# Performance work log

Hardware: AMD Instinct MI355X
Metric: run time of the kernel (lower is better)

## Reference

```python
import jax, jax.numpy as jnp
import numpy as np

N = 84          # nodes; N*(N-1)/2 == 3486, hardcoded by LayerNorm shapes
P = 3486        # number of pairwise rows
H = 2048        # h_size
EPS = 1e-5


def _gru_cell(x, h, Wih, Whh, bih, bhh):
    # PyTorch GRUCell math. Wih: [3H, in], Whh: [3H, H]
    gi = x @ Wih.T + bih
    gh = h @ Whh.T + bhh
    ir, iz, inew = jnp.split(gi, 3, axis=1)
    hr, hz, hnew = jnp.split(gh, 3, axis=1)
    r = jax.nn.sigmoid(ir + hr)
    z = jax.nn.sigmoid(iz + hz)
    n = jnp.tanh(inew + r * hnew)
    return (1.0 - z) * n + z * h


def _full_ln(x, w, b):
    # nn.LayerNorm([3486, h]) normalizes over BOTH dims jointly (biased var)
    mu = jnp.mean(x)
    var = jnp.mean((x - mu) ** 2)
    return (x - mu) * jax.lax.rsqrt(var + EPS) * w + b


def setup_inputs() -> dict:
    key = jax.random.key(0)
    ks = jax.random.split(key, 22)
    f32 = jnp.float32

    def nrm(k, shape, std):
        return jax.random.normal(k, shape, dtype=f32) * std

    h2 = H // 2
    return {
        "x": nrm(ks[0], (N, 64), 1.0),
        "hid": nrm(ks[1], (P, H), 1.0),
        # GRUCell(64, H) parameters
        "gru_Wih": nrm(ks[2], (3 * H, 64), 1.0 / np.sqrt(64)),
        "gru_Whh": nrm(ks[3], (3 * H, H), 1.0 / np.sqrt(H)),
        "gru_bih": nrm(ks[4], (3 * H,), 0.01),
        "gru_bhh": nrm(ks[5], (3 * H,), 0.01),
        # Linear/LayerNorm stack
        "W1": nrm(ks[6], (H, H), np.sqrt(2.0 / H)),
        "b1": jnp.zeros((H,), f32),
        "ln1_w": jnp.ones((P, H), f32),
        "ln1_b": jnp.zeros((P, H), f32),
        "W2": nrm(ks[7], (h2, H), np.sqrt(2.0 / H)),
        "b2": jnp.zeros((h2,), f32),
        "ln2_w": jnp.ones((P, h2), f32),
        "ln2_b": jnp.zeros((P, h2), f32),
        "W3": nrm(ks[8], (h2, h2), np.sqrt(2.0 / h2)),
        "b3": jnp.zeros((h2,), f32),
        "ln3_w": jnp.ones((P, h2), f32),
        "ln3_b": jnp.zeros((P, h2), f32),
        "W4": nrm(ks[9], (1, h2), np.sqrt(2.0 / h2)),
        "b4": jnp.zeros((1,), f32),
    }


def reference(x, hid, gru_Wih, gru_Whh, gru_bih, gru_bhh,
              W1, b1, ln1_w, ln1_b, W2, b2, ln2_w, ln2_b,
              W3, b3, ln3_w, ln3_b, W4, b4):
    # Pairwise gather: rows ordered (0,1),(0,2),...,(0,N-1),(1,2),... -- matches
    # the torch loop of expand+cat.
    iu, ju = jnp.triu_indices(N, k=1)
    x1 = x[iu]  # [P, 64]
    x2 = x[ju]  # [P, 64]

    h = _gru_cell(x1, hid, gru_Wih, gru_Whh, gru_bih, gru_bhh)
    h = _gru_cell(x2, h, gru_Wih, gru_Whh, gru_bih, gru_bhh)

    h = _full_ln(jax.nn.relu(h @ W1.T + b1), ln1_w, ln1_b)
    h = _full_ln(jax.nn.relu(h @ W2.T + b2), ln2_w, ln2_b)
    h = _full_ln(jax.nn.relu(h @ W3.T + b3), ln3_w, ln3_b)
    vals = jax.nn.sigmoid(h @ W4.T + b4)[:, 0]  # [P]

    # Strict-upper-triangular scatter + symmetrize (equals the torch pad loop)
    M = jnp.zeros((N, N), dtype=vals.dtype).at[iu, ju].set(vals)
    return M + M.T
```

## Files before the change

### kernel.cpp

```cpp
#include <hip/hip_runtime.h>
#include <stdint.h>

#define P_PAIRS 3486
#define NNODES 84
#define HSZ 2048
#define H2SZ 1024
#define G3H 6144
#define LN_EPS 1e-5f

typedef short bf16x8 __attribute__((ext_vector_type(8)));
typedef float f32x4 __attribute__((ext_vector_type(4)));

typedef __attribute__((address_space(3))) unsigned int lds_uint;
typedef __attribute__((address_space(1))) const unsigned int global_cuint;

__device__ __forceinline__ unsigned short f2bf(float f) {
    unsigned int u = __float_as_uint(f);
    return (unsigned short)((u + 0x7fffu + ((u >> 16) & 1u)) >> 16);
}
__device__ __forceinline__ float bf2f(unsigned short s) {
    return __uint_as_float(((unsigned int)s) << 16);
}
__device__ __forceinline__ float sigm(float x) {
    return 1.f / (1.f + expf(-x));
}

#define S_WHH (G3H * HSZ / 4)
#define S_W1  (HSZ * HSZ / 4)
#define S_W2  (H2SZ * HSZ / 4)
#define S_W3  (H2SZ * H2SZ / 4)
#define S_HID (P_PAIRS * HSZ / 4)
#define B0 (S_WHH)
#define B1 (B0 + S_W1)
#define B2 (B1 + S_W2)
#define B3 (B2 + S_W3)
#define B4 (B3 + S_HID)

__device__ __forceinline__ void cvt4(const float4* in, ushort4* out, int i) {
    float4 v = in[i];
    ushort4 o;
    o.x = f2bf(v.x); o.y = f2bf(v.y); o.z = f2bf(v.z); o.w = f2bf(v.w);
    out[i] = o;
}

__global__ void k_prep(const float4* __restrict__ Whh, ushort4* __restrict__ whh_b,
                       const float4* __restrict__ W1, ushort4* __restrict__ w1_b,
                       const float4* __restrict__ W2, ushort4* __restrict__ w2_b,
                       const float4* __restrict__ W3, ushort4* __restrict__ w3_b,
                       const float4* __restrict__ hid, ushort4* __restrict__ hid_b,
                       int* __restrict__ ip, int* __restrict__ jp, float* __restrict__ acc) {
    int idx = blockIdx.x * blockDim.x + threadIdx.x;
    if (idx < 8) acc[idx] = 0.f;
    if (idx < P_PAIRS) {
        int i = 0, rem = idx;
        while (rem >= NNODES - 1 - i) { rem -= NNODES - 1 - i; ++i; }
        ip[idx] = i;
        jp[idx] = i + 1 + rem;
    }
    int stride = gridDim.x * blockDim.x;
    for (; idx < B4; idx += stride) {
        if (idx < B0)      cvt4(Whh, whh_b, idx);
        else if (idx < B1) cvt4(W1, w1_b, idx - B0);
        else if (idx < B2) cvt4(W2, w2_b, idx - B1);
        else if (idx < B3) cvt4(W3, w3_b, idx - B2);
        else               cvt4(hid, hid_b, idx - B3);
    }
}

__global__ void k_gi(const float* __restrict__ x, const float* __restrict__ Wih,
                     const float* __restrict__ bih, float* __restrict__ gi) {
    int idx = blockIdx.x * blockDim.x + threadIdx.x;
    if (idx >= NNODES * G3H) return;
    int node = idx / G3H, n = idx - node * G3H;
    const float* xr = x + node * 64;
    const float* wr = Wih + (size_t)n * 64;
    float s = bih[n];
#pragma unroll
    for (int k = 0; k < 64; ++k) s += xr[k] * wr[k];
    gi[idx] = s;
}

__global__ __launch_bounds__(256)
void k_gemm(const unsigned short* __restrict__ A, const unsigned short* __restrict__ B,
            const float* __restrict__ bias, float* __restrict__ C,
            int M, int N, int K, int relu, float* __restrict__ accg, int redslot) {
    __shared__ __align__(16) unsigned short lsA[2 * 128 * 32];
    __shared__ __align__(16) unsigned short lsB[2 * 128 * 32];
    const int m0 = blockIdx.x * 128;
    const int n0 = blockIdx.y * 128;
    const int tid = threadIdx.x;
    const int lane = tid & 63;
    const int wave = tid >> 6;
    const int wr = (wave >> 1) * 64;
    const int wc = (wave & 1) * 64;
    const int fr = lane & 15;
    const int quad = lane >> 4;
    const int kof = quad * 8;

    f32x4 acc[4][4];
#pragma unroll
    for (int i = 0; i < 4; ++i)
#pragma unroll
        for (int j = 0; j < 4; ++j) {
            f32x4 z = {0.f, 0.f, 0.f, 0.f};
            acc[i][j] = z;
        }

    const int lin0 = (wave * 2) * 1024 + lane * 16;
    const int lin1 = lin0 + 1024;
    const int row0 = lin0 >> 6, col0 = (lin0 & 63) >> 1;
    const int row1 = lin1 >> 6, col1 = (lin1 & 63) >> 1;
    int ga0 = m0 + row0; if (ga0 >= M) ga0 = M - 1;
    int ga1 = m0 + row1; if (ga1 >= M) ga1 = M - 1;
    const int gb0 = n0 + row0, gb1 = n0 + row1;

    const unsigned short* pa0 = A + (size_t)ga0 * K + col0;
    const unsigned short* pa1 = A + (size_t)ga1 * K + col1;
    const unsigned short* pb0 = B + (size_t)gb0 * K + col0;
    const unsigned short* pb1 = B + (size_t)gb1 * K + col1;
    const int ch0 = (wave * 2) * 512;
    const int ch1 = ch0 + 512;

    for (int k0 = 0; k0 < K; k0 += 64) {
        __syncthreads();
#pragma unroll
        for (int h = 0; h < 2; ++h) {
            const int ko = k0 + h * 32;
            const int hb = h * 4096;
            __builtin_amdgcn_global_load_lds((global_cuint*)(pa0 + ko), (lds_uint*)&lsA[hb + ch0], 16, 0, 0);
            __builtin_amdgcn_global_load_lds((global_cuint*)(pa1 + ko), (lds_uint*)&lsA[hb + ch1], 16, 0, 0);
            __builtin_amdgcn_global_load_lds((global_cuint*)(pb0 + ko), (lds_uint*)&lsB[hb + ch0], 16, 0, 0);
            __builtin_amdgcn_global_load_lds((global_cuint*)(pb1 + ko), (lds_uint*)&lsB[hb + ch1], 16, 0, 0);
        }
        __syncthreads();
        bf16x8 av[2][4], bv[2][4];
#pragma unroll
        for (int h = 0; h < 2; ++h) {
            const int hb = h * 4096;
#pragma unroll
            for (int mi = 0; mi < 4; ++mi)
                av[h][mi] = *(const bf16x8*)(&lsA[hb + (wr + mi * 16 + fr) * 32 + kof]);
#pragma unroll
            for (int ni = 0; ni < 4; ++ni)
                bv[h][ni] = *(const bf16x8*)(&lsB[hb + (wc + ni * 16 + fr) * 32 + kof]);
        }
#pragma unroll
        for (int h = 0; h < 2; ++h)
#pragma unroll
            for (int mi = 0; mi < 4; ++mi)
#pragma unroll
                for (int ni = 0; ni < 4; ++ni)
                    acc[mi][ni] = __builtin_amdgcn_mfma_f32_16x16x32_bf16(av[h][mi], bv[h][ni], acc[mi][ni], 0, 0, 0);
    }

    float s1 = 0.f, s2 = 0.f;
#pragma unroll
    for (int mi = 0; mi < 4; ++mi) {
#pragma unroll
        for (int r = 0; r < 4; ++r) {
            int row = m0 + wr + mi * 16 + quad * 4 + r;
            if (row >= M) continue;
#pragma unroll
            for (int ni = 0; ni < 4; ++ni) {
                int col = n0 + wc + ni * 16 + fr;
                float v = acc[mi][ni][r];
                if (bias) v += bias[col];
                if (relu) v = fmaxf(v, 0.f);
                if (redslot >= 0) { s1 += v; s2 += v * v; }
                C[(size_t)row * N + col] = v;
            }
        }
    }

    if (redslot >= 0) {
        __syncthreads();
        float* sm = (float*)lsA;
        sm[tid] = s1;
        sm[256 + tid] = s2;
        __syncthreads();
        for (int o = 128; o > 0; o >>= 1) {
            if (tid < o) {
                sm[tid] += sm[tid + o];
                sm[256 + tid] += sm[256 + tid + o];
            }
            __syncthreads();
        }
        if (tid == 0) {
            atomicAdd(&accg[redslot * 2], sm[0]);
            atomicAdd(&accg[redslot * 2 + 1], sm[256]);
        }
    }
}

__global__ void k_combine(const float4* __restrict__ gi, const float4* __restrict__ gh,
                          const int* __restrict__ pair, const float4* __restrict__ hprev_f,
                          const ushort4* __restrict__ hprev_b,
                          ushort4* __restrict__ hout) {
    int idx = blockIdx.x * blockDim.x + threadIdx.x;
    if (idx >= P_PAIRS * (HSZ / 4)) return;
    int p = idx >> 9;
    int c4 = idx & 511;
    int node = pair[p];
    const float4* gip = gi + (size_t)node * (G3H / 4) + c4;
    const float4* ghp = gh + (size_t)p * (G3H / 4) + c4;
    float4 gir = gip[0],   ghr = ghp[0];
    float4 giz = gip[512], ghz = ghp[512];
    float4 gin = gip[1024], ghn = ghp[1024];
    float hp[4];
    if (hprev_f) {
        float4 h = hprev_f[idx];
        hp[0] = h.x; hp[1] = h.y; hp[2] = h.z; hp[3] = h.w;
    } else {
        ushort4 h = hprev_b[idx];
        hp[0] = bf2f(h.x); hp[1] = bf2f(h.y); hp[2] = bf2f(h.z); hp[3] = bf2f(h.w);
    }
    float ir[4] = {gir.x, gir.y, gir.z, gir.w}, hr[4] = {ghr.x, ghr.y, ghr.z, ghr.w};
    float iz[4] = {giz.x, giz.y, giz.z, giz.w}, hz[4] = {ghz.x, ghz.y, ghz.z, ghz.w};
    float in_[4] = {gin.x, gin.y, gin.z, gin.w}, hn[4] = {ghn.x, ghn.y, ghn.z, ghn.w};
    unsigned short o[4];
#pragma unroll
    for (int q = 0; q < 4; ++q) {
        float r = sigm(ir[q] + hr[q]);
        float z = sigm(iz[q] + hz[q]);
        float nn = tanhf(in_[q] + r * hn[q]);
        o[q] = f2bf((1.f - z) * nn + z * hp[q]);
    }
    ushort4 ov = {o[0], o[1], o[2], o[3]};
    hout[idx] = ov;
}

__global__ void k_lnapply(const float4* __restrict__ t, const float4* __restrict__ w,
                          const float4* __restrict__ b, const float* __restrict__ acc, int slot,
                          int n, ushort4* __restrict__ out) {
    float cnt = (float)n;
    float mu = acc[slot * 2] / cnt;
    float var = acc[slot * 2 + 1] / cnt - mu * mu;
    float inv = rsqrtf(var + LN_EPS);
    int n4 = n >> 2;
    int idx = blockIdx.x * blockDim.x + threadIdx.x;
    int stride = gridDim.x * blockDim.x;
    for (; idx < n4; idx += stride) {
        float4 tv = t[idx], wv = w[idx], bv = b[idx];
        ushort4 o;
        o.x = f2bf((tv.x - mu) * inv * wv.x + bv.x);
        o.y = f2bf((tv.y - mu) * inv * wv.y + bv.y);
        o.z = f2bf((tv.z - mu) * inv * wv.z + bv.z);
        o.w = f2bf((tv.w - mu) * inv * wv.w + bv.w);
        out[idx] = o;
    }
}

__global__ void k_head(const float* __restrict__ t, const float* __restrict__ w,
                       const float* __restrict__ b, const float* __restrict__ accv,
                       const float* __restrict__ W4, const float* __restrict__ b4,
                       float* __restrict__ vals) {
    float cnt = (float)P_PAIRS * (float)H2SZ;
    float mu = accv[4] / cnt;
    float var = accv[5] / cnt - mu * mu;
    float inv = rsqrtf(var + LN_EPS);
    int wid = (blockIdx.x * blockDim.x + threadIdx.x) >> 6;
    int lane = threadIdx.x & 63;
    if (wid >= P_PAIRS) return;
    const float* row = t + (size_t)wid * H2SZ;
    const float* wrp = w + (size_t)wid * H2SZ;
    const float* brp = b + (size_t)wid * H2SZ;
    float s = 0.f;
    for (int k = lane; k < H2SZ; k += 64)
        s += ((row[k] - mu) * inv * wrp[k] + brp[k]) * W4[k];
#pragma unroll
    for (int o = 32; o > 0; o >>= 1) s += __shfl_down(s, o, 64);
    if (lane == 0) vals[wid] = sigm(s + b4[0]);
}

__global__ void k_out(const float* __restrict__ vals, float* __restrict__ out) {
    int idx = blockIdx.x * blockDim.x + threadIdx.x;
    if (idx >= NNODES * NNODES) return;
    int r = idx / NNODES, c = idx - r * NNODES;
    if (r == c) { out[idx] = 0.f; return; }
    int i = r < c ? r : c, j = r < c ? c : r;
    int p = i * (NNODES - 1) - i * (i - 1) / 2 + (j - i - 1);
    out[idx] = vals[p];
}

extern "C" void kernel_launch(void* const* d_in, const int* in_sizes, int n_in,
                              void* d_out, int out_size, void* d_ws, size_t ws_size,
                              hipStream_t stream) {
    const float* x    = (const float*)d_in[0];
    const float* hid  = (const float*)d_in[1];
    const float* Wih  = (const float*)d_in[2];
    const float* Whh  = (const float*)d_in[3];
    const float* bih  = (const float*)d_in[4];
    const float* bhh  = (const float*)d_in[5];
    const float* W1   = (const float*)d_in[6];
    const float* b1   = (const float*)d_in[7];
    const float* ln1w = (const float*)d_in[8];
    const float* ln1b = (const float*)d_in[9];
    const float* W2   = (const float*)d_in[10];
    const float* b2   = (const float*)d_in[11];
    const float* ln2w = (const float*)d_in[12];
    const float* ln2b = (const float*)d_in[13];
    const float* W3   = (const float*)d_in[14];
    const float* b3   = (const float*)d_in[15];
    const float* ln3w = (const float*)d_in[16];
    const float* ln3b = (const float*)d_in[17];
    const float* W4   = (const float*)d_in[18];
    const float* b4   = (const float*)d_in[19];
    float* out = (float*)d_out;

    char* ws = (char*)d_ws;
    size_t off = 0;
    auto alloc = [&](size_t bytes) -> void* {
        off = (off + 255) & ~(size_t)255;
        void* p = ws + off;
        off += bytes;
        return p;
    };

    float* acc            = (float*)alloc(8 * sizeof(float));
    int*   ip             = (int*)alloc(P_PAIRS * sizeof(int));
    int*   jp             = (int*)alloc(P_PAIRS * sizeof(int));
    float* gi             = (float*)alloc((size_t)NNODES * G3H * sizeof(float));
    unsigned short* whh_b = (unsigned short*)alloc((size_t)G3H * HSZ * 2);
    unsigned short* w1_b  = (unsigned short*)alloc((size_t)HSZ * HSZ * 2);
    unsigned short* w2_b  = (unsigned short*)alloc((size_t)H2SZ * HSZ * 2);
    unsigned short* w3_b  = (unsigned short*)alloc((size_t)H2SZ * H2SZ * 2);
    unsigned short* hid_b = (unsigned short*)alloc((size_t)P_PAIRS * HSZ * 2);
    unsigned short* hbuf  = (unsigned short*)alloc((size_t)P_PAIRS * HSZ * 2);
    float* gh             = (float*)alloc((size_t)P_PAIRS * G3H * sizeof(float));
    float* vals           = (float*)alloc((size_t)P_PAIRS * sizeof(float));
    (void)ws_size; (void)in_sizes; (void)n_in; (void)out_size;

    float* t = gh;
    unsigned short* lnb = hid_b;

    k_prep<<<2048, 256, 0, stream>>>((const float4*)Whh, (ushort4*)whh_b,
                                     (const float4*)W1, (ushort4*)w1_b,
                                     (const float4*)W2, (ushort4*)w2_b,
                                     (const float4*)W3, (ushort4*)w3_b,
                                     (const float4*)hid, (ushort4*)hid_b,
                                     ip, jp, acc);
    k_gi<<<(NNODES * G3H + 255) / 256, 256, 0, stream>>>(x, Wih, bih, gi);

    dim3 gBig((P_PAIRS + 127) / 128, G3H / 128);
    int cgrid = (P_PAIRS * HSZ / 4 + 255) / 256;
    k_gemm<<<gBig, 256, 0, stream>>>(hid_b, whh_b, bhh, gh, P_PAIRS, G3H, HSZ, 0, acc, -1);
    k_combine<<<cgrid, 256, 0, stream>>>((const float4*)gi, (const float4*)gh, ip,
                                         (const float4*)hid, nullptr, (ushort4*)hbuf);
    k_gemm<<<gBig, 256, 0, stream>>>(hbuf, whh_b, bhh, gh, P_PAIRS, G3H, HSZ, 0, acc, -1);
    k_combine<<<cgrid, 256, 0, stream>>>((const float4*)gi, (const float4*)gh, jp,
                                         nullptr, (const ushort4*)hbuf, (ushort4*)hbuf);

    dim3 g3((P_PAIRS + 127) / 128, HSZ / 128);
    k_gemm<<<g3, 256, 0, stream>>>(hbuf, w1_b, b1, t, P_PAIRS, HSZ, HSZ, 1, acc, 0);
    k_lnapply<<<2048, 256, 0, stream>>>((const float4*)t, (const float4*)ln1w, (const float4*)ln1b,
                                        acc, 0, P_PAIRS * HSZ, (ushort4*)lnb);

    dim3 g4((P_PAIRS + 127) / 128, H2SZ / 128);
    k_gemm<<<g4, 256, 0, stream>>>(lnb, w2_b, b2, t, P_PAIRS, H2SZ, HSZ, 1, acc, 1);
    k_lnapply<<<2048, 256, 0, stream>>>((const float4*)t, (const float4*)ln2w, (const float4*)ln2b,
                                        acc, 1, P_PAIRS * H2SZ, (ushort4*)lnb);

    k_gemm<<<g4, 256, 0, stream>>>(lnb, w3_b, b3, t, P_PAIRS, H2SZ, H2SZ, 1, acc, 2);

    k_head<<<(P_PAIRS * 64 + 255) / 256, 256, 0, stream>>>(t, ln3w, ln3b, acc, W4, b4, vals);

    k_out<<<(NNODES * NNODES + 255) / 256, 256, 0, stream>>>(vals, out);
}
```

Measured before the change: 781.0 us.

## Store GRU hidden GEMM output in bf16, swizzle GEMM tiles, shrink K step

The GRU hidden-projection GEMM now writes its result as bf16 instead of fp32, which halves the write and read traffic of the large gh buffer consumed by the combine kernel. The GEMM grid becomes 1D with grouped tile ordering (8 N-tiles per group) to improve L2 reuse of the weight tiles. The K loop step is reduced from 64 to 32 with half the LDS, which doubles barrier count but may raise occupancy. Storing gate pre-activations in bf16 costs some precision, and the separate t buffer adds workspace.

```diff
diff --git a/kernel.cpp b/kernel.cpp
--- a/kernel.cpp
+++ b/kernel.cpp
@@ -82,12 +82,19 @@
 
 __global__ __launch_bounds__(256)
 void k_gemm(const unsigned short* __restrict__ A, const unsigned short* __restrict__ B,
-            const float* __restrict__ bias, float* __restrict__ C,
+            const float* __restrict__ bias, float* __restrict__ Cf,
+            unsigned short* __restrict__ Cb,
             int M, int N, int K, int relu, float* __restrict__ accg, int redslot) {
-    __shared__ __align__(16) unsigned short lsA[2 * 128 * 32];
-    __shared__ __align__(16) unsigned short lsB[2 * 128 * 32];
-    const int m0 = blockIdx.x * 128;
-    const int n0 = blockIdx.y * 128;
+    __shared__ __align__(16) unsigned short lsA[128 * 32];
+    __shared__ __align__(16) unsigned short lsB[128 * 32];
+    const int mt_count = (M + 127) >> 7;
+    const int per_group = mt_count << 3;
+    const int g = blockIdx.x / per_group;
+    const int rr = blockIdx.x - g * per_group;
+    const int nt = (g << 3) + (rr & 7);
+    const int mt = rr >> 3;
+    const int m0 = mt * 128;
+    const int n0 = nt * 128;
     const int tid = threadIdx.x;
     const int lane = tid & 63;
     const int wave = tid >> 6;
@@ -118,39 +125,30 @@
     const unsigned short* pa1 = A + (size_t)ga1 * K + col1;
     const unsigned short* pb0 = B + (size_t)gb0 * K + col0;
     const unsigned short* pb1 = B + (size_t)gb1 * K + col1;
-    const int ch0 = (wave * 2) * 512;
-    const int ch1 = ch0 + 512;
-
-    for (int k0 = 0; k0 < K; k0 += 64) {
+    lds_uint* la0 = (lds_uint*)&lsA[(wave * 2) * 512];
+    lds_uint* la1 = (lds_uint*)&lsA[(wave * 2 + 1) * 512];
+    lds_uint* lb0 = (lds_uint*)&lsB[(wave * 2) * 512];
+    lds_uint* lb1 = (lds_uint*)&lsB[(wave * 2 + 1) * 512];
+
+    for (int k0 = 0; k0 < K; k0 += 32) {
         __syncthreads();
-#pragma unroll
-        for (int h = 0; h < 2; ++h) {
-            const int ko = k0 + h * 32;
-            const int hb = h * 4096;
-            __builtin_amdgcn_global_load_lds((global_cuint*)(pa0 + ko), (lds_uint*)&lsA[hb + ch0], 16, 0, 0);
-            __builtin_amdgcn_global_load_lds((global_cuint*)(pa1 + ko), (lds_uint*)&lsA[hb + ch1], 16, 0, 0);
-            __builtin_amdgcn_global_load_lds((global_cuint*)(pb0 + ko), (lds_uint*)&lsB[hb + ch0], 16, 0, 0);
-            __builtin_amdgcn_global_load_lds((global_cuint*)(pb1 + ko), (lds_uint*)&lsB[hb + ch1], 16, 0, 0);
-        }
+        __builtin_amdgcn_global_load_lds((global_cuint*)(pa0 + k0), la0, 16, 0, 0);
+        __builtin_amdgcn_global_load_lds((global_cuint*)(pa1 + k0), la1, 16, 0, 0);
+        __builtin_amdgcn_global_load_lds((global_cuint*)(pb0 + k0), lb0, 16, 0, 0);
+        __builtin_amdgcn_global_load_lds((global_cuint*)(pb1 + k0), lb1, 16, 0, 0);
         __syncthreads();
-        bf16x8 av[2][4], bv[2][4];
-#pragma unroll
-        for (int h = 0; h < 2; ++h) {
-            const int hb = h * 4096;
-#pragma unroll
-            for (int mi = 0; mi < 4; ++mi)
-                av[h][mi] = *(const bf16x8*)(&lsA[hb + (wr + mi * 16 + fr) * 32 + kof]);
+        bf16x8 av[4], bv[4];
+#pragma unroll
+        for (int mi = 0; mi < 4; ++mi)
+            av[mi] = *(const bf16x8*)(&lsA[(wr + mi * 16 + fr) * 32 + kof]);
+#pragma unroll
+        for (int ni = 0; ni < 4; ++ni)
+            bv[ni] = *(const bf16x8*)(&lsB[(wc + ni * 16 + fr) * 32 + kof]);
+#pragma unroll
+        for (int mi = 0; mi < 4; ++mi)
 #pragma unroll
             for (int ni = 0; ni < 4; ++ni)
-                bv[h][ni] = *(const bf16x8*)(&lsB[hb + (wc + ni * 16 + fr) * 32 + kof]);
-        }
-#pragma unroll
-        for (int h = 0; h < 2; ++h)
-#pragma unroll
-            for (int mi = 0; mi < 4; ++mi)
-#pragma unroll
-                for (int ni = 0; ni < 4; ++ni)
-                    acc[mi][ni] = __builtin_amdgcn_mfma_f32_16x16x32_bf16(av[h][mi], bv[h][ni], acc[mi][ni], 0, 0, 0);
+                acc[mi][ni] = __builtin_amdgcn_mfma_f32_16x16x32_bf16(av[mi], bv[ni], acc[mi][ni], 0, 0, 0);
     }
 
     float s1 = 0.f, s2 = 0.f;
@@ -167,7 +165,8 @@
                 if (bias) v += bias[col];
                 if (relu) v = fmaxf(v, 0.f);
                 if (redslot >= 0) { s1 += v; s2 += v * v; }
-                C[(size_t)row * N + col] = v;
+                if (Cb) Cb[(size_t)row * N + col] = f2bf(v);
+                else    Cf[(size_t)row * N + col] = v;
             }
         }
     }
@@ -192,7 +191,7 @@
     }
 }
 
-__global__ void k_combine(const float4* __restrict__ gi, const float4* __restrict__ gh,
+__global__ void k_combine(const float4* __restrict__ gi, const ushort4* __restrict__ gh,
                           const int* __restrict__ pair, const float4* __restrict__ hprev_f,
                           const ushort4* __restrict__ hprev_b,
                           ushort4* __restrict__ hout) {
@@ -202,10 +201,12 @@
     int c4 = idx & 511;
     int node = pair[p];
     const float4* gip = gi + (size_t)node * (G3H / 4) + c4;
-    const float4* ghp = gh + (size_t)p * (G3H / 4) + c4;
-    float4 gir = gip[0],   ghr = ghp[0];
-    float4 giz = gip[512], ghz = ghp[512];
-    float4 gin = gip[1024], ghn = ghp[1024];
+    const ushort4* ghp = gh + (size_t)p * (G3H / 4) + c4;
+    float4 gir = gip[0],   giz = gip[512], gin = gip[1024];
+    ushort4 ghr4 = ghp[0], ghz4 = ghp[512], ghn4 = ghp[1024];
+    float hr[4] = {bf2f(ghr4.x), bf2f(ghr4.y), bf2f(ghr4.z), bf2f(ghr4.w)};
+    float hz[4] = {bf2f(ghz4.x), bf2f(ghz4.y), bf2f(ghz4.z), bf2f(ghz4.w)};
+    float hn[4] = {bf2f(ghn4.x), bf2f(ghn4.y), bf2f(ghn4.z), bf2f(ghn4.w)};
     float hp[4];
     if (hprev_f) {
         float4 h = hprev_f[idx];
@@ -214,9 +215,9 @@
         ushort4 h = hprev_b[idx];
         hp[0] = bf2f(h.x); hp[1] = bf2f(h.y); hp[2] = bf2f(h.z); hp[3] = bf2f(h.w);
     }
-    float ir[4] = {gir.x, gir.y, gir.z, gir.w}, hr[4] = {ghr.x, ghr.y, ghr.z, ghr.w};
-    float iz[4] = {giz.x, giz.y, giz.z, giz.w}, hz[4] = {ghz.x, ghz.y, ghz.z, ghz.w};
-    float in_[4] = {gin.x, gin.y, gin.z, gin.w}, hn[4] = {ghn.x, ghn.y, ghn.z, ghn.w};
+    float ir[4] = {gir.x, gir.y, gir.z, gir.w};
+    float iz[4] = {giz.x, giz.y, giz.z, giz.w};
+    float in_[4] = {gin.x, gin.y, gin.z, gin.w};
     unsigned short o[4];
 #pragma unroll
     for (int q = 0; q < 4; ++q) {
@@ -326,11 +327,11 @@
     unsigned short* w3_b  = (unsigned short*)alloc((size_t)H2SZ * H2SZ * 2);
     unsigned short* hid_b = (unsigned short*)alloc((size_t)P_PAIRS * HSZ * 2);
     unsigned short* hbuf  = (unsigned short*)alloc((size_t)P_PAIRS * HSZ * 2);
-    float* gh             = (float*)alloc((size_t)P_PAIRS * G3H * sizeof(float));
+    unsigned short* gh    = (unsigned short*)alloc((size_t)P_PAIRS * G3H * 2);
+    float* t              = (float*)alloc((size_t)P_PAIRS * HSZ * sizeof(float));
     float* vals           = (float*)alloc((size_t)P_PAIRS * sizeof(float));
     (void)ws_size; (void)in_sizes; (void)n_in; (void)out_size;
 
-    float* t = gh;
     unsigned short* lnb = hid_b;
 
     k_prep<<<2048, 256, 0, stream>>>((const float4*)Whh, (ushort4*)whh_b,
@@ -341,26 +342,28 @@
                                      ip, jp, acc);
     k_gi<<<(NNODES * G3H + 255) / 256, 256, 0, stream>>>(x, Wih, bih, gi);
 
-    dim3 gBig((P_PAIRS + 127) / 128, G3H / 128);
+    const int MT = (P_PAIRS + 127) / 128;
+    int gBig = MT * (G3H / 128);
+    int g3   = MT * (HSZ / 128);
+    int g4   = MT * (H2SZ / 128);
     int cgrid = (P_PAIRS * HSZ / 4 + 255) / 256;
-    k_gemm<<<gBig, 256, 0, stream>>>(hid_b, whh_b, bhh, gh, P_PAIRS, G3H, HSZ, 0, acc, -1);
-    k_combine<<<cgrid, 256, 0, stream>>>((const float4*)gi, (const float4*)gh, ip,
+
+    k_gemm<<<gBig, 256, 0, stream>>>(hid_b, whh_b, bhh, nullptr, gh, P_PAIRS, G3H, HSZ, 0, acc, -1);
+    k_combine<<<cgrid, 256, 0, stream>>>((const float4*)gi, (const ushort4*)gh, ip,
                                          (const float4*)hid, nullptr, (ushort4*)hbuf);
-    k_gemm<<<gBig, 256, 0, stream>>>(hbuf, whh_b, bhh, gh, P_PAIRS, G3H, HSZ, 0, acc, -1);
-    k_combine<<<cgrid, 256, 0, stream>>>((const float4*)gi, (const float4*)gh, jp,
+    k_gemm<<<gBig, 256, 0, stream>>>(hbuf, whh_b, bhh, nullptr, gh, P_PAIRS, G3H, HSZ, 0, acc, -1);
+    k_combine<<<cgrid, 256, 0, stream>>>((const float4*)gi, (const ushort4*)gh, jp,
                                          nullptr, (const ushort4*)hbuf, (ushort4*)hbuf);
 
-    dim3 g3((P_PAIRS + 127) / 128, HSZ / 128);
-    k_gemm<<<g3, 256, 0, stream>>>(hbuf, w1_b, b1, t, P_PAIRS, HSZ, HSZ, 1, acc, 0);
+    k_gemm<<<g3, 256, 0, stream>>>(hbuf, w1_b, b1, t, nullptr, P_PAIRS, HSZ, HSZ, 1, acc, 0);
     k_lnapply<<<2048, 256, 0, stream>>>((const float4*)t, (const float4*)ln1w, (const float4*)ln1b,
                                         acc, 0, P_PAIRS * HSZ, (ushort4*)lnb);
 
-    dim3 g4((P_PAIRS + 127) / 128, H2SZ / 128);
-    k_gemm<<<g4, 256, 0, stream>>>(lnb, w2_b, b2, t, P_PAIRS, H2SZ, HSZ, 1, acc, 1);
+    k_gemm<<<g4, 256, 0, stream>>>(lnb, w2_b, b2, t, nullptr, P_PAIRS, H2SZ, HSZ, 1, acc, 1);
     k_lnapply<<<2048, 256, 0, stream>>>((const float4*)t, (const float4*)ln2w, (const float4*)ln2b,
                                         acc, 1, P_PAIRS * H2SZ, (ushort4*)lnb);
 
-    k_gemm<<<g4, 256, 0, stream>>>(lnb, w3_b, b3, t, P_PAIRS, H2SZ, H2SZ, 1, acc, 2);
+    k_gemm<<<g4, 256, 0, stream>>>(lnb, w3_b, b3, t, nullptr, P_PAIRS, H2SZ, H2SZ, 1, acc, 2);
 
     k_head<<<(P_PAIRS * 64 + 255) / 256, 256, 0, stream>>>(t, ln3w, ln3b, acc, W4, b4, vals);
 
```

Result: slower. 839.7 us (+7.5%).
